# Kernel optimization log

Hardware: AMD Instinct MI355X
Metric: run time of the kernel (lower is better)

## Reference

```python
import jax, jax.numpy as jnp
import numpy as np

N, E, H = 25000, 100000, 32          # nodes, edges, node/clique hidden dim
NC, A, EC = 8000, 50000, 24000       # cliques, node2clique assignments, clique edges
EEMB, CEE, L = 8, 8, 2               # edge emb dims, n layers


def segment_mean(vals, ids, num):
    s = jax.ops.segment_sum(vals, ids, num_segments=num)
    cnt = jax.ops.segment_sum(jnp.ones(ids.shape[0], vals.dtype), ids, num_segments=num)
    return s / jnp.maximum(cnt, 1.0)[:, None]


def setup_inputs() -> dict:
    key = jax.random.key(0)
    ks = jax.random.split(key, 24)
    s = 0.1  # param scale
    inp = {
        "node_features": jax.random.normal(ks[0], (N, H), jnp.float32),
        "edge_index": jax.random.randint(ks[1], (2, E), 0, N),
        "edge_features": jax.random.normal(ks[2], (E, EEMB), jnp.float32),
        "clique_features": jax.random.normal(ks[3], (NC, H), jnp.float32),
        "node2clique_index": jnp.stack([
            jax.random.randint(ks[4], (A,), 0, N),
            jax.random.randint(ks[5], (A,), 0, NC)]),
        "clique_edge_index": jax.random.randint(ks[6], (2, EC), 0, NC),
        "clique_edge_features": jax.random.normal(ks[7], (EC, CEE), jnp.float32),
        # node NNConv params (stacked over L layers)
        "nn1_w": jax.random.normal(ks[8], (L, EEMB, H)) * s,
        "nn1_b": jnp.zeros((L, H)),
        "nn2_w": jax.random.normal(ks[9], (L, H, H * H)) * s,
        "nn2_b": jnp.zeros((L, H * H)),
        "root_w": jax.random.normal(ks[10], (L, H, H)) * s,
        "root_b": jnp.zeros((L, H)),
        # Node2Clique linear
        "n2c_w": jax.random.normal(ks[11], (L, H, H)) * s,
        "n2c_b": jnp.zeros((L, H)),
        # clique NNConv params
        "cnn1_w": jax.random.normal(ks[12], (L, CEE, H)) * s,
        "cnn1_b": jnp.zeros((L, H)),
        "cnn2_w": jax.random.normal(ks[13], (L, H, H * H)) * s,
        "cnn2_b": jnp.zeros((L, H * H)),
        "croot_w": jax.random.normal(ks[14], (L, H, H)) * s,
        "croot_b": jnp.zeros((L, H)),
        # Clique2Node linear
        "c2n_w": jax.random.normal(ks[15], (L, H, H)) * s,
        "c2n_b": jnp.zeros((L, H)),
    }
    return inp


def nnconv(x, src, dst, edge_attr, w1, b1, w2, b2, rw, rb, n_out_nodes):
    # per-edge weight matrices from the edge MLP: [E, in, out]
    h = jax.nn.relu(edge_attr @ w1 + b1)
    We = (h @ w2 + b2).reshape(edge_attr.shape[0], x.shape[1], -1)
    msg = jnp.einsum('ei,eio->eo', x[src], We)           # message from source
    agg = segment_mean(msg, dst, n_out_nodes)            # mean aggregation at target
    return agg + x @ rw + rb                             # root weight + bias


def reference(node_features, edge_index, edge_features, clique_features,
              node2clique_index, clique_edge_index, clique_edge_features,
              nn1_w, nn1_b, nn2_w, nn2_b, root_w, root_b, n2c_w, n2c_b,
              cnn1_w, cnn1_b, cnn2_w, cnn2_b, croot_w, croot_b, c2n_w, c2n_b):
    x, c = node_features, clique_features
    src, dst = edge_index[0], edge_index[1]
    nid, cid = node2clique_index[0], node2clique_index[1]
    csrc, cdst = clique_edge_index[0], clique_edge_index[1]
    for l in range(L):
        # node-level edge-conditioned conv
        x = jax.nn.relu(nnconv(x, src, dst, edge_features,
                               nn1_w[l], nn1_b[l], nn2_w[l], nn2_b[l],
                               root_w[l], root_b[l], N))
        # Node2Clique: project node feats, scatter-mean into cliques
        m = x @ n2c_w[l] + n2c_b[l]
        c = c + segment_mean(m[nid], cid, NC)
        # clique-level edge-conditioned conv
        c = jax.nn.relu(nnconv(c, csrc, cdst, clique_edge_features,
                               cnn1_w[l], cnn1_b[l], cnn2_w[l], cnn2_b[l],
                               croot_w[l], croot_b[l], NC))
        # Clique2Node: project clique feats, scatter-mean back onto nodes
        m = c @ c2n_w[l] + c2n_b[l]
        x = x + segment_mean(m[cid], nid, N)
    return (x, c)
```

## Files before the change

kernel.cpp:

```cpp
#include <hip/hip_runtime.h>
#include <hip/hip_bf16.h>

typedef unsigned int u32;
typedef unsigned short u16;

#define DEVINL __device__ __forceinline__

constexpr int Nn  = 25000;
constexpr int Ee  = 100000;
constexpr int NCc = 8000;
constexpr int Aa  = 50000;
constexpr int ECc = 24000;
constexpr int TCOLS = 1088;
constexpr int WPSZ  = TCOLS*32;
constexpr int TSP   = 1064;
constexpr int NB_N = (Nn + 255)/256;
constexpr int NB_C = (NCc + 255)/256;

typedef float f32x4 __attribute__((ext_vector_type(4)));
typedef short s16x8 __attribute__((ext_vector_type(8)));

DEVINL float b2f(u16 u){ union{u32 i;float f;}v; v.i = ((u32)u)<<16; return v.f; }
DEVINL float bfl(u32 u){ union{u32 i;float f;}v; v.i = u<<16; return v.f; }
DEVINL float bfh(u32 u){ union{u32 i;float f;}v; v.i = u & 0xffff0000u; return v.f; }
DEVINL u16 f2b(float f){ union{float f;u32 i;}v; v.f=f; u32 i=v.i;
  return (u16)((i + 0x7fffu + ((i>>16)&1u)) >> 16); }
DEVINL float ldw(const void* p, long i, int f){
  return f ? ((const float*)p)[i] : b2f(((const u16*)p)[i]);
}

__global__ __launch_bounds__(256) void k_detect(const u16* __restrict__ p, int n,
                        u32* __restrict__ maxbits, int* __restrict__ zcnt,
                        int* __restrict__ done, int* __restrict__ flag){
  int i0 = blockIdx.x*256 + threadIdx.x;
  float lm = 0.f; int lz = 0;
  for (int i = i0; i < n; i += gridDim.x*256){
    u16 v = p[i];
    if (v == 0) lz++;
    lm = fmaxf(lm, fabsf(b2f(v)));
  }
  #pragma unroll
  for (int off = 32; off; off >>= 1){
    lm = fmaxf(lm, __shfl_down(lm, off));
    lz += __shfl_down(lz, off);
  }
  if ((threadIdx.x & 63) == 0){
    atomicMax(maxbits, __float_as_uint(lm));
    atomicAdd(zcnt, lz);
  }
  __syncthreads();
  if (threadIdx.x == 0){
    __threadfence();
    if (atomicAdd(done, 1) == gridDim.x - 1){
      float m = __uint_as_float(*maxbits);
      *flag = (m > 1e6f || *zcnt > n/4) ? 1 : 0;
    }
  }
}

__global__ __launch_bounds__(256) void k_conv_all(const void* __restrict__ xin, const void* __restrict__ cin,
                         float* __restrict__ xA, float* __restrict__ cA, const int* __restrict__ flag){
  int i = blockIdx.x*256 + threadIdx.x;
  int f = *flag;
  if (i < Nn*32) xA[i] = ldw(xin, i, f);
  else { i -= Nn*32; if (i < NCc*32) cA[i] = ldw(cin, i, f); }
}

__global__ __launch_bounds__(256) void k_count_all(const int* __restrict__ ei, const int* __restrict__ cei,
                          const int* __restrict__ n2c,
                          int* __restrict__ deg_nd, int* __restrict__ deg_ce,
                          int* __restrict__ deg_n2c, int* __restrict__ deg_c2n,
                          int* __restrict__ cnt_sn, int* __restrict__ cnt_sc){
  int i = blockIdx.x*256 + threadIdx.x;
  if (i < Ee)                             atomicAdd(&deg_nd[ei[Ee + i]], 1);
  else if ((i -= Ee) < ECc)               atomicAdd(&deg_ce[cei[ECc + i]], 1);
  else if ((i -= ECc) < Aa)               atomicAdd(&deg_n2c[n2c[Aa + i]], 1);
  else if ((i -= Aa) < Aa)                atomicAdd(&deg_c2n[n2c[i]], 1);
  else if ((i -= Aa) < Ee)                atomicAdd(&cnt_sn[ei[i]], 1);
  else if ((i -= Ee) < ECc)               atomicAdd(&cnt_sc[cei[i]], 1);
}

__global__ __launch_bounds__(256) void k_scan_block(const int* __restrict__ cnt_n, const int* __restrict__ cnt_c,
                           int* __restrict__ offs_n, int* __restrict__ offs_c,
                           int* __restrict__ bsum_n, int* __restrict__ bsum_c){
  __shared__ int s[256];
  bool isC = blockIdx.x >= NB_N;
  int bid = isC ? blockIdx.x - NB_N : blockIdx.x;
  const int* cnt = isC ? cnt_c : cnt_n;
  int M = isC ? NCc : Nn;
  int tid = threadIdx.x;
  int i = bid*256 + tid;
  int v = (i < M) ? cnt[i] : 0;
  s[tid] = v; __syncthreads();
  for (int d = 1; d < 256; d <<= 1){
    int t = (tid >= d) ? s[tid-d] : 0;
    __syncthreads();
    s[tid] += t;
    __syncthreads();
  }
  if (i < M) (isC ? offs_c : offs_n)[i] = s[tid] - v;
  if (tid == 255) (isC ? bsum_c : bsum_n)[bid] = s[255];
}

__global__ __launch_bounds__(256) void k_spine(int* __restrict__ bn, int* __restrict__ bc){
  __shared__ int s[256];
  int tid = threadIdx.x;
  int v;
  if (tid < 128) v = (tid < NB_N) ? bn[tid] : 0;
  else           v = (tid-128 < NB_C) ? bc[tid-128] : 0;
  s[tid] = v; __syncthreads();
  for (int d = 1; d < 128; d <<= 1){
    int lane = tid & 127;
    int t = (lane >= d) ? s[tid-d] : 0;
    __syncthreads();
    s[tid] += t;
    __syncthreads();
  }
  if (tid < NB_N) bn[tid] = s[tid] - v;
  else if (tid >= 128 && tid-128 < NB_C) bc[tid-128] = s[tid] - v;
}

__global__ __launch_bounds__(256) void k_scan_fix(int* __restrict__ offs_n, int* __restrict__ offs_c,
                         const int* __restrict__ bn, const int* __restrict__ bc){
  int i = blockIdx.x*256 + threadIdx.x;
  if (i < Nn) offs_n[i] += bn[i >> 8];
  else if ((i -= Nn) < NCc) offs_c[i] += bc[i >> 8];
}

__global__ __launch_bounds__(256) void k_place(const int* __restrict__ ei, const int* __restrict__ cei,
                      const int* __restrict__ offs_n, const int* __restrict__ offs_c,
                      int* __restrict__ cur_n, int* __restrict__ cur_c,
                      int* __restrict__ perm_n, int* __restrict__ perm_c){
  int i = blockIdx.x*256 + threadIdx.x;
  if (i < Ee){
    int s = ei[i];
    perm_n[offs_n[s] + atomicAdd(&cur_n[s], 1)] = i;
  } else if ((i -= Ee) < ECc){
    int s = cei[i];
    perm_c[offs_c[s] + atomicAdd(&cur_c[s], 1)] = i;
  }
}

__global__ __launch_bounds__(256) void k_gather(const int* __restrict__ ei, const int* __restrict__ cei,
                       const int* __restrict__ perm_n, const int* __restrict__ perm_c,
                       const void* __restrict__ ef, const void* __restrict__ cef,
                       const int* __restrict__ flag,
                       int2* __restrict__ sdp_n, float* __restrict__ efp_n,
                       int2* __restrict__ sdp_c, float* __restrict__ efp_c){
  int i = blockIdx.x*256 + threadIdx.x;
  int f = *flag;
  if (i < Ee*8){
    int p = i >> 3, j = i & 7;
    int e = perm_n[p];
    efp_n[i] = ldw(ef, (long)e*8 + j, f);
    if (j == 0) sdp_n[p] = make_int2(ei[e], ei[Ee + e]);
  } else if ((i -= Ee*8) < ECc*8){
    int p = i >> 3, j = i & 7;
    int e = perm_c[p];
    efp_c[i] = ldw(cef, (long)e*8 + j, f);
    if (j == 0) sdp_c[p] = make_int2(cei[e], cei[ECc + e]);
  }
}

__global__ __launch_bounds__(256) void k_wpack_all(const void* __restrict__ nn2w, const void* __restrict__ nn2b,
                          const void* __restrict__ rootw,
                          const void* __restrict__ cnn2w, const void* __restrict__ cnn2b,
                          const void* __restrict__ crootw,
                          const int* __restrict__ flag, u16* __restrict__ Wp4){
  int i = blockIdx.x*256 + threadIdx.x;
  if (i >= 4*WPSZ) return;
  int set = i / WPSZ, j = i - set*WPSZ;
  int l = set >> 1, isC = set & 1;
  const void* W2 = isC ? cnn2w : nn2w;
  const void* B2 = isC ? cnn2b : nn2b;
  const void* RW = isC ? crootw : rootw;
  int f = *flag;
  int col = j >> 5, ii = j & 31;
  float v;
  if (col < 1024)      v = ldw(W2, (long)l*32768 + ((col>>5)<<10) + (ii<<5) + (col&31), f);
  else if (col < 1056) v = ldw(B2, (long)l*1024 + (ii<<5) + (col-1024), f);
  else                 v = ldw(RW, (long)l*1024 + (ii<<5) + (col-1056), f);
  Wp4[i] = f2b(v);
}

__global__ __launch_bounds__(512) void k_conv_fused(const float* __restrict__ base,
                           const float* __restrict__ addagg, const int* __restrict__ adddeg, int M,
                           const int2* __restrict__ sdp, const float* __restrict__ efp,
                           const int* __restrict__ offs, int E_,
                           const void* __restrict__ w1, long w1off,
                           const void* __restrict__ b1, long b1off,
                           const u16* __restrict__ Wp,
                           const void* __restrict__ rb, long rboff,
                           const int* __restrict__ flag,
                           float* __restrict__ feat_root, float* __restrict__ agg){
  __shared__ __align__(16) u16 Ts[16*TSP];
  __shared__ float w1s[256], b1s[32];
  __shared__ u32 hws[8][4][16];
  int tid = threadIdx.x;
  int w = tid >> 6, lane = tid & 63;
  int quad = lane >> 4, lm = lane & 15;
  int n0 = blockIdx.x * 16;
  int f = *flag;
  if (tid < 256) w1s[tid] = ldw(w1, w1off + tid, f);
  else if (tid < 288) b1s[tid-256] = ldw(b1, b1off + (tid-256), f);
  int n = n0 + lm;
  int nc = n < M ? n : M-1;
  const float* bp = base + (size_t)nc*32 + quad*8;
  s16x8 bfrag;
  if (addagg){
    int dg = adddeg[nc];
    float d = (float)(dg > 1 ? dg : 1);
    const float* ap = addagg + (size_t)nc*32 + quad*8;
    #pragma unroll
    for (int j = 0; j < 8; j++) bfrag[j] = (short)f2b(bp[j] + ap[j]/d);
  } else {
    #pragma unroll
    for (int j = 0; j < 8; j++) bfrag[j] = (short)f2b(bp[j]);
  }
  #pragma unroll 1
  for (int ti = 0; ti < 9; ti++){
    int ct = w*9 + ti;
    if (ct >= 68) break;
    int colbase = ct*16;
    s16x8 afrag = *(const s16x8*)(Wp + (size_t)(colbase + lm)*32 + quad*8);
    f32x4 acc = {0.f, 0.f, 0.f, 0.f};
    acc = __builtin_amdgcn_mfma_f32_16x16x32_bf16(afrag, bfrag, acc, 0, 0, 0);
    int cb = colbase + quad*4;
    if (ct < 66){
      u32 lo = (u32)f2b(acc[0]) | ((u32)f2b(acc[1]) << 16);
      u32 hi = (u32)f2b(acc[2]) | ((u32)f2b(acc[3]) << 16);
      *(uint2*)&Ts[lm*TSP + cb] = make_uint2(lo, hi);
    } else if (n < M){
      int o = cb - 1056;
      float4 v = make_float4(acc[0] + ldw(rb, rboff+o,   f),
                             acc[1] + ldw(rb, rboff+o+1, f),
                             acc[2] + ldw(rb, rboff+o+2, f),
                             acc[3] + ldw(rb, rboff+o+3, f));
      *(float4*)&feat_root[(size_t)n*32 + o] = v;
    }
  }
  __syncthreads();
  int lo = offs[n0];
  int n1 = n0 + 16;
  int hi = (n1 < M) ? offs[n1] : E_;
  int eg = quad, kk = lm;
  int pos = lo + w*4;
  float efv = 0.f; int sdv = 0;
  if (lane < 32){ int idx = pos*8 + lane; if (idx < hi*8) efv = efp[idx]; }
  else if (lane < 40){ int idx = pos*2 + (lane-32); if (idx < hi*2) sdv = ((const int*)sdp)[idx]; }
  for (; pos < hi; pos += 32){
    int np = pos + 32;
    float efv_n = 0.f; int sdv_n = 0;
    if (lane < 32){ int idx = np*8 + lane; if (idx < hi*8) efv_n = efp[idx]; }
    else if (lane < 40){ int idx = np*2 + (lane-32); if (idx < hi*2) sdv_n = ((const int*)sdp)[idx]; }
    int sn = __shfl(sdv, 32 + 2*eg);
    int dn = __shfl(sdv, 33 + 2*eg);
    bool valid = (pos + eg < hi);
    int sr = sn - n0; sr = sr < 0 ? 0 : (sr > 15 ? 15 : sr);
    float a0 = b1s[2*kk], a1 = b1s[2*kk+1];
    #pragma unroll
    for (int j = 0; j < 8; j++){
      float ev = __shfl(efv, eg*8 + j);
      a0 += ev * w1s[j*32 + 2*kk];
      a1 += ev * w1s[j*32 + 2*kk+1];
    }
    hws[w][eg][kk] = (u32)f2b(fmaxf(a0, 0.f)) | ((u32)f2b(fmaxf(a1, 0.f)) << 16);
    if (valid){
      const u16* Tr = &Ts[sr*TSP];
      u32 vb = *(const u32*)&Tr[1024 + 2*kk];
      float m0 = bfl(vb), m1 = bfh(vb);
      #pragma unroll
      for (int kq = 0; kq < 16; kq++){
        u32 hp = hws[w][eg][kq];
        float h0 = bfl(hp), h1 = bfh(hp);
        u32 v0 = *(const u32*)&Tr[(2*kq)*32 + 2*kk];
        u32 v1 = *(const u32*)&Tr[(2*kq+1)*32 + 2*kk];
        m0 += h0*bfl(v0) + h1*bfl(v1);
        m1 += h0*bfh(v0) + h1*bfh(v1);
      }
      float* ap = agg + (size_t)dn*32 + 2*kk;
      atomicAdd(ap,   m0);
      atomicAdd(ap+1, m1);
    }
    efv = efv_n; sdv = sdv_n;
  }
}

__global__ __launch_bounds__(256) void k_update_lin(const float* __restrict__ agg, const int* __restrict__ deg,
                           const float* __restrict__ feat_root, int M,
                           const void* __restrict__ w, long woff,
                           const void* __restrict__ b, long boff,
                           const int* __restrict__ flag,
                           float* __restrict__ feat, float* __restrict__ m_out){
  __shared__ float wsm[1024], bs[32], rows[8][33];
  int tid = threadIdx.x;
  int f = *flag;
  for (int idx = tid; idx < 1024; idx += 256) wsm[idx] = ldw(w, woff + idx, f);
  if (tid < 32) bs[tid] = ldw(b, boff + tid, f);
  int nl = tid >> 5, o = tid & 31;
  int n = blockIdx.x*8 + nl;
  if (n < M){
    int dg = deg[n];
    float d = (float)(dg > 1 ? dg : 1);
    float v = fmaxf(agg[(size_t)n*32 + o]/d + feat_root[(size_t)n*32 + o], 0.f);
    rows[nl][o] = v;
    feat[(size_t)n*32 + o] = v;
  }
  __syncthreads();
  if (n >= M) return;
  float acc = bs[o];
  #pragma unroll
  for (int j = 0; j < 32; j++) acc += rows[nl][j]*wsm[j*32+o];
  m_out[(size_t)n*32 + o] = acc;
}

__global__ __launch_bounds__(256) void k_scatter(const int* __restrict__ gidx, const int* __restrict__ sidx, int A_,
                          const float* __restrict__ m, float* __restrict__ agg){
  int i = blockIdx.x*256 + threadIdx.x;
  if (i >= A_*32) return;
  int a = i >> 5, o = i & 31;
  atomicAdd(&agg[(size_t)sidx[a]*32 + o], m[(size_t)gidx[a]*32 + o]);
}

__global__ __launch_bounds__(256) void k_store(const float* __restrict__ x, const float* __restrict__ xagg,
                      const int* __restrict__ xdeg, const float* __restrict__ c,
                      void* __restrict__ out, const int* __restrict__ flag){
  int i = blockIdx.x*256 + threadIdx.x;
  int tot = Nn*32 + NCc*32;
  if (i >= tot) return;
  float v;
  if (i < Nn*32){
    int n = i >> 5;
    int dg = xdeg[n];
    float d = (float)(dg > 1 ? dg : 1);
    v = x[i] + xagg[i]/d;
  } else v = c[i - Nn*32];
  if (*flag) ((float*)out)[i] = v;
  else       ((u16*)out)[i]   = f2b(v);
}

extern "C" void kernel_launch(void* const* d_in, const int* in_sizes, int n_in,
                              void* d_out, int out_size, void* d_ws, size_t ws_size,
                              hipStream_t stream){
  const int* ei  = (const int*)d_in[1];
  const int* n2c = (const int*)d_in[4];
  const int* cei = (const int*)d_in[5];
  const void *efr = d_in[2], *cefr = d_in[6];
  const void *nn1w = d_in[7], *nn1b = d_in[8], *nn2w = d_in[9], *nn2b = d_in[10],
             *rootw = d_in[11], *rootb = d_in[12], *n2cw = d_in[13], *n2cb = d_in[14],
             *cnn1w = d_in[15], *cnn1b = d_in[16], *cnn2w = d_in[17], *cnn2b = d_in[18],
             *crootw = d_in[19], *crootb = d_in[20], *c2nw = d_in[21], *c2nb = d_in[22];

  char* ws = (char*)d_ws;
  size_t off = 0;
  auto alloc = [&](size_t bytes){ void* p = ws + off; off += (bytes + 255) & ~(size_t)255; return p; };

  size_t zstart = off;
  float *aggE[2], *caggS[2], *caggE[2], *aggS[2];
  for (int l = 0; l < 2; l++){
    aggE[l]  = (float*)alloc((size_t)Nn*32*4);
    caggS[l] = (float*)alloc((size_t)NCc*32*4);
    caggE[l] = (float*)alloc((size_t)NCc*32*4);
    aggS[l]  = (float*)alloc((size_t)Nn*32*4);
  }
  int* deg_nd  = (int*)alloc((size_t)Nn*4);
  int* deg_ce  = (int*)alloc((size_t)NCc*4);
  int* deg_n2c = (int*)alloc((size_t)NCc*4);
  int* deg_c2n = (int*)alloc((size_t)Nn*4);
  int* cnt_sn  = (int*)alloc((size_t)Nn*4);
  int* cnt_sc  = (int*)alloc((size_t)NCc*4);
  int* cur_n   = (int*)alloc((size_t)Nn*4);
  int* cur_c   = (int*)alloc((size_t)NCc*4);
  u32* maxbits = (u32*)alloc(256);
  int* zcnt = (int*)((char*)maxbits + 4);
  int* flag = (int*)((char*)maxbits + 8);
  int* done = (int*)((char*)maxbits + 12);
  size_t zbytes = off - zstart;

  float* xA  = (float*)alloc((size_t)Nn*32*4);
  float* xB  = (float*)alloc((size_t)Nn*32*4);
  float* xC  = (float*)alloc((size_t)Nn*32*4);
  float* cA  = (float*)alloc((size_t)NCc*32*4);
  float* cC0 = (float*)alloc((size_t)NCc*32*4);
  float* cC1 = (float*)alloc((size_t)NCc*32*4);
  float* m   = (float*)alloc((size_t)Nn*32*4);
  float* frn = (float*)alloc((size_t)Nn*32*4);
  float* frc = (float*)alloc((size_t)NCc*32*4);
  int* offs_n = (int*)alloc((size_t)Nn*4);
  int* offs_c = (int*)alloc((size_t)NCc*4);
  int* bsum_n = (int*)alloc(512);
  int* bsum_c = (int*)alloc(512);
  int* perm_n = (int*)alloc((size_t)Ee*4);
  int* perm_c = (int*)alloc((size_t)ECc*4);
  int2* sdp_n = (int2*)alloc((size_t)Ee*8);
  int2* sdp_c = (int2*)alloc((size_t)ECc*8);
  float* efp_n = (float*)alloc((size_t)Ee*8*4);
  float* efp_c = (float*)alloc((size_t)ECc*8*4);
  u16* Wp4 = (u16*)alloc((size_t)4*WPSZ*2);

  auto nb = [](int n){ return (n + 255)/256; };

  hipMemsetAsync(ws + zstart, 0, zbytes, stream);
  k_detect<<<256,256,0,stream>>>((const u16*)d_in[0], Nn*32, maxbits, zcnt, done, flag);
  k_conv_all<<<nb(Nn*32 + NCc*32),256,0,stream>>>(d_in[0], d_in[3], xA, cA, flag);
  k_count_all<<<nb(2*Ee + 2*ECc + 2*Aa),256,0,stream>>>(ei, cei, n2c,
      deg_nd, deg_ce, deg_n2c, deg_c2n, cnt_sn, cnt_sc);
  k_scan_block<<<NB_N+NB_C,256,0,stream>>>(cnt_sn, cnt_sc, offs_n, offs_c, bsum_n, bsum_c);
  k_spine<<<1,256,0,stream>>>(bsum_n, bsum_c);
  k_scan_fix<<<nb(Nn+NCc),256,0,stream>>>(offs_n, offs_c, bsum_n, bsum_c);
  k_place<<<nb(Ee+ECc),256,0,stream>>>(ei, cei, offs_n, offs_c, cur_n, cur_c, perm_n, perm_c);
  k_gather<<<nb(8*(Ee+ECc)),256,0,stream>>>(ei, cei, perm_n, perm_c, efr, cefr, flag,
      sdp_n, efp_n, sdp_c, efp_c);
  k_wpack_all<<<nb(4*WPSZ),256,0,stream>>>(nn2w, nn2b, rootw, cnn2w, cnn2b, crootw, flag, Wp4);

  int Gn = (Nn + 15)/16, Gc = (NCc + 15)/16;

  k_conv_fused<<<Gn,512,0,stream>>>(xA, nullptr, nullptr, Nn, sdp_n, efp_n, offs_n, Ee,
      nn1w, 0, nn1b, 0, Wp4 + 0*WPSZ, rootb, 0, flag, frn, aggE[0]);
  k_update_lin<<<(Nn+7)/8,256,0,stream>>>(aggE[0], deg_nd, frn, Nn, n2cw, 0, n2cb, 0, flag, xB, m);
  k_scatter<<<nb(Aa*32),256,0,stream>>>(n2c, n2c+Aa, Aa, m, caggS[0]);
  k_conv_fused<<<Gc,512,0,stream>>>(cA, caggS[0], deg_n2c, NCc, sdp_c, efp_c, offs_c, ECc,
      cnn1w, 0, cnn1b, 0, Wp4 + 1*WPSZ, crootb, 0, flag, frc, caggE[0]);
  k_update_lin<<<(NCc+7)/8,256,0,stream>>>(caggE[0], deg_ce, frc, NCc, c2nw, 0, c2nb, 0, flag, cC0, m);
  k_scatter<<<nb(Aa*32),256,0,stream>>>(n2c+Aa, n2c, Aa, m, aggS[0]);
  k_conv_fused<<<Gn,512,0,stream>>>(xB, aggS[0], deg_c2n, Nn, sdp_n, efp_n, offs_n, Ee,
      nn1w, 256, nn1b, 32, Wp4 + 2*WPSZ, rootb, 32, flag, frn, aggE[1]);
  k_update_lin<<<(Nn+7)/8,256,0,stream>>>(aggE[1], deg_nd, frn, Nn, n2cw, 1024, n2cb, 32, flag, xC, m);
  k_scatter<<<nb(Aa*32),256,0,stream>>>(n2c, n2c+Aa, Aa, m, caggS[1]);
  k_conv_fused<<<Gc,512,0,stream>>>(cC0, caggS[1], deg_n2c, NCc, sdp_c, efp_c, offs_c, ECc,
      cnn1w, 256, cnn1b, 32, Wp4 + 3*WPSZ, crootb, 32, flag, frc, caggE[1]);
  k_update_lin<<<(NCc+7)/8,256,0,stream>>>(caggE[1], deg_ce, frc, NCc, c2nw, 1024, c2nb, 32, flag, cC1, m);
  k_scatter<<<nb(Aa*32),256,0,stream>>>(n2c+Aa, n2c, Aa, m, aggS[1]);
  k_store<<<nb(Nn*32 + NCc*32),256,0,stream>>>(xC, aggS[1], deg_c2n, cC1, d_out, flag);
}
```

Before: 347.3 us.

## Replace atomic scatter-mean with CSR segment-mean and restructure conv smem layout

Builds CSR indices for node-to-clique and clique-to-node assignments (extra scan segments and placement) so the scatter-mean steps become deterministic gather-based segment means with no atomics. Those kernels also apply the residual add, which removes the add-aggregate path from the conv kernel. The conv kernel's shared-memory tile is re-laid out as packed u32 with a new stride, allowing 128-bit vector reads in the message loop. Edge-feature prefetch is deepened to two iterations ahead. In exchange there is more preprocessing work, and the per-thread serial loops in the segment-mean kernels may suffer from load imbalance.

```diff
diff --git a/kernel.cpp b/kernel.cpp
--- a/kernel.cpp
+++ b/kernel.cpp
@@ -13,7 +13,7 @@
 constexpr int ECc = 24000;
 constexpr int TCOLS = 1088;
 constexpr int WPSZ  = TCOLS*32;
-constexpr int TSP   = 1064;
+constexpr int NSTR  = 580;
 constexpr int NB_N = (Nn + 255)/256;
 constexpr int NB_C = (NCc + 255)/256;
 
@@ -25,6 +25,7 @@
 DEVINL float bfh(u32 u){ union{u32 i;float f;}v; v.i = u & 0xffff0000u; return v.f; }
 DEVINL u16 f2b(float f){ union{float f;u32 i;}v; v.f=f; u32 i=v.i;
   return (u16)((i + 0x7fffu + ((i>>16)&1u)) >> 16); }
+DEVINL u32 pk2(float a, float b){ return (u32)f2b(a) | ((u32)f2b(b) << 16); }
 DEVINL float ldw(const void* p, long i, int f){
   return f ? ((const float*)p)[i] : b2f(((const u16*)p)[i]);
 }
@@ -80,16 +81,23 @@
   else if ((i -= Ee) < ECc)               atomicAdd(&cnt_sc[cei[i]], 1);
 }
 
-__global__ __launch_bounds__(256) void k_scan_block(const int* __restrict__ cnt_n, const int* __restrict__ cnt_c,
-                           int* __restrict__ offs_n, int* __restrict__ offs_c,
-                           int* __restrict__ bsum_n, int* __restrict__ bsum_c){
+__global__ __launch_bounds__(256) void k_scan_block(
+    const int* __restrict__ c0, const int* __restrict__ c1,
+    const int* __restrict__ c2, const int* __restrict__ c3,
+    int* __restrict__ o0, int* __restrict__ o1, int* __restrict__ o2, int* __restrict__ o3,
+    int* __restrict__ b0, int* __restrict__ b1, int* __restrict__ b2, int* __restrict__ b3){
   __shared__ int s[256];
-  bool isC = blockIdx.x >= NB_N;
-  int bid = isC ? blockIdx.x - NB_N : blockIdx.x;
-  const int* cnt = isC ? cnt_c : cnt_n;
-  int M = isC ? NCc : Nn;
+  int bid = blockIdx.x, seg, rb;
+  if (bid < NB_N){ seg=0; rb=bid; }
+  else if (bid < NB_N+NB_C){ seg=1; rb=bid-NB_N; }
+  else if (bid < 2*NB_N+NB_C){ seg=2; rb=bid-NB_N-NB_C; }
+  else { seg=3; rb=bid-2*NB_N-NB_C; }
+  const int* cnt = seg==0?c0 : seg==1?c1 : seg==2?c2 : c3;
+  int* offs = seg==0?o0 : seg==1?o1 : seg==2?o2 : o3;
+  int* bs   = seg==0?b0 : seg==1?b1 : seg==2?b2 : b3;
+  int M = (seg & 1) ? NCc : Nn;
   int tid = threadIdx.x;
-  int i = bid*256 + tid;
+  int i = rb*256 + tid;
   int v = (i < M) ? cnt[i] : 0;
   s[tid] = v; __syncthreads();
   for (int d = 1; d < 256; d <<= 1){
@@ -98,39 +106,46 @@
     s[tid] += t;
     __syncthreads();
   }
-  if (i < M) (isC ? offs_c : offs_n)[i] = s[tid] - v;
-  if (tid == 255) (isC ? bsum_c : bsum_n)[bid] = s[255];
-}
-
-__global__ __launch_bounds__(256) void k_spine(int* __restrict__ bn, int* __restrict__ bc){
-  __shared__ int s[256];
-  int tid = threadIdx.x;
-  int v;
-  if (tid < 128) v = (tid < NB_N) ? bn[tid] : 0;
-  else           v = (tid-128 < NB_C) ? bc[tid-128] : 0;
+  if (i < M) offs[i] = s[tid] - v;
+  if (tid == 255) bs[rb] = s[255];
+}
+
+__global__ __launch_bounds__(512) void k_spine(int* __restrict__ b0, int* __restrict__ b1,
+                      int* __restrict__ b2, int* __restrict__ b3){
+  __shared__ int s[512];
+  int tid = threadIdx.x, seg = tid >> 7, lane = tid & 127;
+  int NB = (seg & 1) ? NB_C : NB_N;
+  int* bp = seg==0?b0 : seg==1?b1 : seg==2?b2 : b3;
+  int v = (lane < NB) ? bp[lane] : 0;
   s[tid] = v; __syncthreads();
   for (int d = 1; d < 128; d <<= 1){
-    int lane = tid & 127;
     int t = (lane >= d) ? s[tid-d] : 0;
     __syncthreads();
     s[tid] += t;
     __syncthreads();
   }
-  if (tid < NB_N) bn[tid] = s[tid] - v;
-  else if (tid >= 128 && tid-128 < NB_C) bc[tid-128] = s[tid] - v;
-}
-
-__global__ __launch_bounds__(256) void k_scan_fix(int* __restrict__ offs_n, int* __restrict__ offs_c,
-                         const int* __restrict__ bn, const int* __restrict__ bc){
-  int i = blockIdx.x*256 + threadIdx.x;
-  if (i < Nn) offs_n[i] += bn[i >> 8];
-  else if ((i -= Nn) < NCc) offs_c[i] += bc[i >> 8];
+  if (lane < NB) bp[lane] = s[tid] - v;
+}
+
+__global__ __launch_bounds__(256) void k_scan_fix(
+    int* __restrict__ o0, int* __restrict__ o1, int* __restrict__ o2, int* __restrict__ o3,
+    const int* __restrict__ b0, const int* __restrict__ b1,
+    const int* __restrict__ b2, const int* __restrict__ b3){
+  int i = blockIdx.x*256 + threadIdx.x;
+  if (i < Nn) o0[i] += b0[i >> 8];
+  else if ((i -= Nn) < NCc) o1[i] += b1[i >> 8];
+  else if ((i -= NCc) < Nn) o2[i] += b2[i >> 8];
+  else if ((i -= Nn) < NCc) o3[i] += b3[i >> 8];
 }
 
 __global__ __launch_bounds__(256) void k_place(const int* __restrict__ ei, const int* __restrict__ cei,
+                      const int* __restrict__ n2c,
                       const int* __restrict__ offs_n, const int* __restrict__ offs_c,
+                      const int* __restrict__ offs_an, const int* __restrict__ offs_ac,
                       int* __restrict__ cur_n, int* __restrict__ cur_c,
-                      int* __restrict__ perm_n, int* __restrict__ perm_c){
+                      int* __restrict__ cur_an, int* __restrict__ cur_ac,
+                      int* __restrict__ perm_n, int* __restrict__ perm_c,
+                      int* __restrict__ an2c, int* __restrict__ ac2n){
   int i = blockIdx.x*256 + threadIdx.x;
   if (i < Ee){
     int s = ei[i];
@@ -138,6 +153,12 @@
   } else if ((i -= Ee) < ECc){
     int s = cei[i];
     perm_c[offs_c[s] + atomicAdd(&cur_c[s], 1)] = i;
+  } else if ((i -= ECc) < Aa){
+    int c = n2c[Aa + i];
+    an2c[offs_ac[c] + atomicAdd(&cur_ac[c], 1)] = n2c[i];
+  } else if ((i -= Aa) < Aa){
+    int nd = n2c[i];
+    ac2n[offs_an[nd] + atomicAdd(&cur_an[nd], 1)] = n2c[Aa + i];
   }
 }
 
@@ -183,8 +204,7 @@
   Wp4[i] = f2b(v);
 }
 
-__global__ __launch_bounds__(512) void k_conv_fused(const float* __restrict__ base,
-                           const float* __restrict__ addagg, const int* __restrict__ adddeg, int M,
+__global__ __launch_bounds__(512) void k_conv_fused(const float* __restrict__ base, int M,
                            const int2* __restrict__ sdp, const float* __restrict__ efp,
                            const int* __restrict__ offs, int E_,
                            const void* __restrict__ w1, long w1off,
@@ -193,30 +213,23 @@
                            const void* __restrict__ rb, long rboff,
                            const int* __restrict__ flag,
                            float* __restrict__ feat_root, float* __restrict__ agg){
-  __shared__ __align__(16) u16 Ts[16*TSP];
-  __shared__ float w1s[256], b1s[32];
-  __shared__ u32 hws[8][4][16];
+  __shared__ __align__(16) u32 Ts[16*NSTR];
+  __shared__ float w1s[256];
+  __shared__ __align__(8) u32 hws[8][4][16];
   int tid = threadIdx.x;
   int w = tid >> 6, lane = tid & 63;
   int quad = lane >> 4, lm = lane & 15;
   int n0 = blockIdx.x * 16;
   int f = *flag;
   if (tid < 256) w1s[tid] = ldw(w1, w1off + tid, f);
-  else if (tid < 288) b1s[tid-256] = ldw(b1, b1off + (tid-256), f);
+  float bb0 = ldw(b1, b1off + 2*lm, f);
+  float bb1 = ldw(b1, b1off + 2*lm + 1, f);
   int n = n0 + lm;
   int nc = n < M ? n : M-1;
   const float* bp = base + (size_t)nc*32 + quad*8;
   s16x8 bfrag;
-  if (addagg){
-    int dg = adddeg[nc];
-    float d = (float)(dg > 1 ? dg : 1);
-    const float* ap = addagg + (size_t)nc*32 + quad*8;
-    #pragma unroll
-    for (int j = 0; j < 8; j++) bfrag[j] = (short)f2b(bp[j] + ap[j]/d);
-  } else {
-    #pragma unroll
-    for (int j = 0; j < 8; j++) bfrag[j] = (short)f2b(bp[j]);
-  }
+  #pragma unroll
+  for (int j = 0; j < 8; j++) bfrag[j] = (short)f2b(bp[j]);
   #pragma unroll 1
   for (int ti = 0; ti < 9; ti++){
     int ct = w*9 + ti;
@@ -225,13 +238,15 @@
     s16x8 afrag = *(const s16x8*)(Wp + (size_t)(colbase + lm)*32 + quad*8);
     f32x4 acc = {0.f, 0.f, 0.f, 0.f};
     acc = __builtin_amdgcn_mfma_f32_16x16x32_bf16(afrag, bfrag, acc, 0, 0, 0);
-    int cb = colbase + quad*4;
     if (ct < 66){
-      u32 lo = (u32)f2b(acc[0]) | ((u32)f2b(acc[1]) << 16);
-      u32 hi = (u32)f2b(acc[2]) | ((u32)f2b(acc[3]) << 16);
-      *(uint2*)&Ts[lm*TSP + cb] = make_uint2(lo, hi);
+      int k = ct >> 1;
+      int p0 = (ct & 1)*8 + quad*2;
+      int idx = lm*NSTR + p0*36 + k;
+      Ts[idx]      = pk2(acc[0], acc[1]);
+      Ts[idx + 36] = pk2(acc[2], acc[3]);
     } else if (n < M){
-      int o = cb - 1056;
+      int o = (ct - 66)*16 + quad*4 - 0;
+      o = (colbase + quad*4) - 1056;
       float4 v = make_float4(acc[0] + ldw(rb, rboff+o,   f),
                              acc[1] + ldw(rb, rboff+o+1, f),
                              acc[2] + ldw(rb, rboff+o+2, f),
@@ -241,48 +256,51 @@
   }
   __syncthreads();
   int lo = offs[n0];
-  int n1 = n0 + 16;
-  int hi = (n1 < M) ? offs[n1] : E_;
+  int hi = (n0 + 16 < M) ? offs[n0 + 16] : E_;
   int eg = quad, kk = lm;
   int pos = lo + w*4;
-  float efv = 0.f; int sdv = 0;
-  if (lane < 32){ int idx = pos*8 + lane; if (idx < hi*8) efv = efp[idx]; }
-  else if (lane < 40){ int idx = pos*2 + (lane-32); if (idx < hi*2) sdv = ((const int*)sdp)[idx]; }
+  float ef0 = 0.f, ef1 = 0.f; int sd0 = 0, sd1 = 0;
+  if (lane < 32){
+    int idx = pos*8 + lane;        if (idx < hi*8) ef0 = efp[idx];
+    idx = (pos+32)*8 + lane;       if (idx < hi*8) ef1 = efp[idx];
+  } else if (lane < 40){
+    int idx = pos*2 + (lane-32);   if (idx < hi*2) sd0 = ((const int*)sdp)[idx];
+    idx = (pos+32)*2 + (lane-32);  if (idx < hi*2) sd1 = ((const int*)sdp)[idx];
+  }
   for (; pos < hi; pos += 32){
-    int np = pos + 32;
-    float efv_n = 0.f; int sdv_n = 0;
-    if (lane < 32){ int idx = np*8 + lane; if (idx < hi*8) efv_n = efp[idx]; }
-    else if (lane < 40){ int idx = np*2 + (lane-32); if (idx < hi*2) sdv_n = ((const int*)sdp)[idx]; }
-    int sn = __shfl(sdv, 32 + 2*eg);
-    int dn = __shfl(sdv, 33 + 2*eg);
+    int np = pos + 64;
+    float ef2 = 0.f; int sd2 = 0;
+    if (lane < 32){ int idx = np*8 + lane; if (idx < hi*8) ef2 = efp[idx]; }
+    else if (lane < 40){ int idx = np*2 + (lane-32); if (idx < hi*2) sd2 = ((const int*)sdp)[idx]; }
+    int sn = __shfl(sd0, 32 + 2*eg);
+    int dn = __shfl(sd0, 33 + 2*eg);
     bool valid = (pos + eg < hi);
     int sr = sn - n0; sr = sr < 0 ? 0 : (sr > 15 ? 15 : sr);
-    float a0 = b1s[2*kk], a1 = b1s[2*kk+1];
+    float a0 = bb0, a1 = bb1;
     #pragma unroll
     for (int j = 0; j < 8; j++){
-      float ev = __shfl(efv, eg*8 + j);
+      float ev = __shfl(ef0, eg*8 + j);
       a0 += ev * w1s[j*32 + 2*kk];
       a1 += ev * w1s[j*32 + 2*kk+1];
     }
-    hws[w][eg][kk] = (u32)f2b(fmaxf(a0, 0.f)) | ((u32)f2b(fmaxf(a1, 0.f)) << 16);
+    hws[w][eg][kk] = pk2(fmaxf(a0, 0.f), fmaxf(a1, 0.f));
     if (valid){
-      const u16* Tr = &Ts[sr*TSP];
-      u32 vb = *(const u32*)&Tr[1024 + 2*kk];
+      const u32* Tr = &Ts[sr*NSTR + kk*36];
+      u32 vb = Tr[32];
       float m0 = bfl(vb), m1 = bfh(vb);
       #pragma unroll
-      for (int kq = 0; kq < 16; kq++){
-        u32 hp = hws[w][eg][kq];
-        float h0 = bfl(hp), h1 = bfh(hp);
-        u32 v0 = *(const u32*)&Tr[(2*kq)*32 + 2*kk];
-        u32 v1 = *(const u32*)&Tr[(2*kq+1)*32 + 2*kk];
-        m0 += h0*bfl(v0) + h1*bfl(v1);
-        m1 += h0*bfh(v0) + h1*bfh(v1);
+      for (int g = 0; g < 8; g++){
+        uint4 tv = *(const uint4*)&Tr[g*4];
+        uint2 hp = *(const uint2*)&hws[w][eg][g*2];
+        float h0 = bfl(hp.x), h1 = bfh(hp.x), h2 = bfl(hp.y), h3 = bfh(hp.y);
+        m0 += h0*bfl(tv.x) + h1*bfl(tv.y) + h2*bfl(tv.z) + h3*bfl(tv.w);
+        m1 += h0*bfh(tv.x) + h1*bfh(tv.y) + h2*bfh(tv.z) + h3*bfh(tv.w);
       }
       float* ap = agg + (size_t)dn*32 + 2*kk;
       atomicAdd(ap,   m0);
       atomicAdd(ap+1, m1);
     }
-    efv = efv_n; sdv = sdv_n;
+    ef0 = ef1; sd0 = sd1; ef1 = ef2; sd1 = sd2;
   }
 }
 
@@ -291,7 +309,8 @@
                            const void* __restrict__ w, long woff,
                            const void* __restrict__ b, long boff,
                            const int* __restrict__ flag,
-                           float* __restrict__ feat, float* __restrict__ m_out){
+                           float* __restrict__ feat, void* __restrict__ dt_out, long dt_off,
+                           float* __restrict__ m_out){
   __shared__ float wsm[1024], bs[32], rows[8][33];
   int tid = threadIdx.x;
   int f = *flag;
@@ -299,42 +318,49 @@
   if (tid < 32) bs[tid] = ldw(b, boff + tid, f);
   int nl = tid >> 5, o = tid & 31;
   int n = blockIdx.x*8 + nl;
+  long i = (long)n*32 + o;
   if (n < M){
     int dg = deg[n];
     float d = (float)(dg > 1 ? dg : 1);
-    float v = fmaxf(agg[(size_t)n*32 + o]/d + feat_root[(size_t)n*32 + o], 0.f);
+    float v = fmaxf(agg[i]/d + feat_root[i], 0.f);
     rows[nl][o] = v;
-    feat[(size_t)n*32 + o] = v;
+    if (feat) feat[i] = v;
+    if (dt_out){
+      if (f) ((float*)dt_out)[dt_off + i] = v;
+      else   ((u16*)dt_out)[dt_off + i]   = f2b(v);
+    }
   }
   __syncthreads();
   if (n >= M) return;
   float acc = bs[o];
   #pragma unroll
   for (int j = 0; j < 32; j++) acc += rows[nl][j]*wsm[j*32+o];
-  m_out[(size_t)n*32 + o] = acc;
-}
-
-__global__ __launch_bounds__(256) void k_scatter(const int* __restrict__ gidx, const int* __restrict__ sidx, int A_,
-                          const float* __restrict__ m, float* __restrict__ agg){
-  int i = blockIdx.x*256 + threadIdx.x;
-  if (i >= A_*32) return;
-  int a = i >> 5, o = i & 31;
-  atomicAdd(&agg[(size_t)sidx[a]*32 + o], m[(size_t)gidx[a]*32 + o]);
-}
-
-__global__ __launch_bounds__(256) void k_store(const float* __restrict__ x, const float* __restrict__ xagg,
-                      const int* __restrict__ xdeg, const float* __restrict__ c,
-                      void* __restrict__ out, const int* __restrict__ flag){
-  int i = blockIdx.x*256 + threadIdx.x;
-  int tot = Nn*32 + NCc*32;
-  if (i >= tot) return;
-  float v;
-  if (i < Nn*32){
-    int n = i >> 5;
-    int dg = xdeg[n];
-    float d = (float)(dg > 1 ? dg : 1);
-    v = x[i] + xagg[i]/d;
-  } else v = c[i - Nn*32];
+  m_out[i] = acc;
+}
+
+__global__ __launch_bounds__(256) void k_segmean(const float* __restrict__ base, const float* __restrict__ m,
+                        const int* __restrict__ idxarr, const int* __restrict__ offs,
+                        const int* __restrict__ deg, int M, float* __restrict__ out){
+  int i = blockIdx.x*256 + threadIdx.x;
+  if (i >= M*32) return;
+  int c = i >> 5, o = i & 31;
+  int lo = offs[c], cnt = deg[c];
+  float s = 0.f;
+  for (int a = lo; a < lo + cnt; a++) s += m[(size_t)idxarr[a]*32 + o];
+  out[i] = base[i] + s/(float)(cnt > 1 ? cnt : 1);
+}
+
+__global__ __launch_bounds__(256) void k_segmean_out(const float* __restrict__ base, const float* __restrict__ m,
+                        const int* __restrict__ idxarr, const int* __restrict__ offs,
+                        const int* __restrict__ deg, int M,
+                        void* __restrict__ out, const int* __restrict__ flag){
+  int i = blockIdx.x*256 + threadIdx.x;
+  if (i >= M*32) return;
+  int c = i >> 5, o = i & 31;
+  int lo = offs[c], cnt = deg[c];
+  float s = 0.f;
+  for (int a = lo; a < lo + cnt; a++) s += m[(size_t)idxarr[a]*32 + o];
+  float v = base[i] + s/(float)(cnt > 1 ? cnt : 1);
   if (*flag) ((float*)out)[i] = v;
   else       ((u16*)out)[i]   = f2b(v);
 }
@@ -356,13 +382,10 @@
   auto alloc = [&](size_t bytes){ void* p = ws + off; off += (bytes + 255) & ~(size_t)255; return p; };
 
   size_t zstart = off;
-  float *aggE[2], *caggS[2], *caggE[2], *aggS[2];
-  for (int l = 0; l < 2; l++){
-    aggE[l]  = (float*)alloc((size_t)Nn*32*4);
-    caggS[l] = (float*)alloc((size_t)NCc*32*4);
-    caggE[l] = (float*)alloc((size_t)NCc*32*4);
-    aggS[l]  = (float*)alloc((size_t)Nn*32*4);
-  }
+  float* aggE0  = (float*)alloc((size_t)Nn*32*4);
+  float* aggE1  = (float*)alloc((size_t)Nn*32*4);
+  float* caggE0 = (float*)alloc((size_t)NCc*32*4);
+  float* caggE1 = (float*)alloc((size_t)NCc*32*4);
   int* deg_nd  = (int*)alloc((size_t)Nn*4);
   int* deg_ce  = (int*)alloc((size_t)NCc*4);
   int* deg_n2c = (int*)alloc((size_t)NCc*4);
@@ -371,6 +394,8 @@
   int* cnt_sc  = (int*)alloc((size_t)NCc*4);
   int* cur_n   = (int*)alloc((size_t)Nn*4);
   int* cur_c   = (int*)alloc((size_t)NCc*4);
+  int* cur_an  = (int*)alloc((size_t)Nn*4);
+  int* cur_ac  = (int*)alloc((size_t)NCc*4);
   u32* maxbits = (u32*)alloc(256);
   int* zcnt = (int*)((char*)maxbits + 4);
   int* flag = (int*)((char*)maxbits + 8);
@@ -379,19 +404,28 @@
 
   float* xA  = (float*)alloc((size_t)Nn*32*4);
   float* xB  = (float*)alloc((size_t)Nn*32*4);
+  float* xA1 = (float*)alloc((size_t)Nn*32*4);
   float* xC  = (float*)alloc((size_t)Nn*32*4);
   float* cA  = (float*)alloc((size_t)NCc*32*4);
+  float* cB  = (float*)alloc((size_t)NCc*32*4);
   float* cC0 = (float*)alloc((size_t)NCc*32*4);
-  float* cC1 = (float*)alloc((size_t)NCc*32*4);
-  float* m   = (float*)alloc((size_t)Nn*32*4);
+  float* cB1 = (float*)alloc((size_t)NCc*32*4);
+  float* m_n = (float*)alloc((size_t)Nn*32*4);
+  float* m_c = (float*)alloc((size_t)NCc*32*4);
   float* frn = (float*)alloc((size_t)Nn*32*4);
   float* frc = (float*)alloc((size_t)NCc*32*4);
-  int* offs_n = (int*)alloc((size_t)Nn*4);
-  int* offs_c = (int*)alloc((size_t)NCc*4);
-  int* bsum_n = (int*)alloc(512);
-  int* bsum_c = (int*)alloc(512);
+  int* offs_n  = (int*)alloc((size_t)Nn*4);
+  int* offs_c  = (int*)alloc((size_t)NCc*4);
+  int* offs_an = (int*)alloc((size_t)Nn*4);
+  int* offs_ac = (int*)alloc((size_t)NCc*4);
+  int* bsum0 = (int*)alloc(512);
+  int* bsum1 = (int*)alloc(512);
+  int* bsum2 = (int*)alloc(512);
+  int* bsum3 = (int*)alloc(512);
   int* perm_n = (int*)alloc((size_t)Ee*4);
   int* perm_c = (int*)alloc((size_t)ECc*4);
+  int* an2c = (int*)alloc((size_t)Aa*4);
+  int* ac2n = (int*)alloc((size_t)Aa*4);
   int2* sdp_n = (int2*)alloc((size_t)Ee*8);
   int2* sdp_c = (int2*)alloc((size_t)ECc*8);
   float* efp_n = (float*)alloc((size_t)Ee*8*4);
@@ -405,31 +439,37 @@
   k_conv_all<<<nb(Nn*32 + NCc*32),256,0,stream>>>(d_in[0], d_in[3], xA, cA, flag);
   k_count_all<<<nb(2*Ee + 2*ECc + 2*Aa),256,0,stream>>>(ei, cei, n2c,
       deg_nd, deg_ce, deg_n2c, deg_c2n, cnt_sn, cnt_sc);
-  k_scan_block<<<NB_N+NB_C,256,0,stream>>>(cnt_sn, cnt_sc, offs_n, offs_c, bsum_n, bsum_c);
-  k_spine<<<1,256,0,stream>>>(bsum_n, bsum_c);
-  k_scan_fix<<<nb(Nn+NCc),256,0,stream>>>(offs_n, offs_c, bsum_n, bsum_c);
-  k_place<<<nb(Ee+ECc),256,0,stream>>>(ei, cei, offs_n, offs_c, cur_n, cur_c, perm_n, perm_c);
+  k_scan_block<<<2*(NB_N+NB_C),256,0,stream>>>(cnt_sn, cnt_sc, deg_c2n, deg_n2c,
+      offs_n, offs_c, offs_an, offs_ac, bsum0, bsum1, bsum2, bsum3);
+  k_spine<<<1,512,0,stream>>>(bsum0, bsum1, bsum2, bsum3);
+  k_scan_fix<<<nb(2*(Nn+NCc)),256,0,stream>>>(offs_n, offs_c, offs_an, offs_ac,
+      bsum0, bsum1, bsum2, bsum3);
+  k_place<<<nb(Ee+ECc+2*Aa),256,0,stream>>>(ei, cei, n2c, offs_n, offs_c, offs_an, offs_ac,
+      cur_n, cur_c, cur_an, cur_ac, perm_n, perm_c, an2c, ac2n);
   k_gather<<<nb(8*(Ee+ECc)),256,0,stream>>>(ei, cei, perm_n, perm_c, efr, cefr, flag,
       sdp_n, efp_n, sdp_c, efp_c);
   k_wpack_all<<<nb(4*WPSZ),256,0,stream>>>(nn2w, nn2b, rootw, cnn2w, cnn2b, crootw, flag, Wp4);
 
   int Gn = (Nn + 15)/16, Gc = (NCc + 15)/16;
 
-  k_conv_fused<<<Gn,512,0,stream>>>(xA, nullptr, nullptr, Nn, sdp_n, efp_n, offs_n, Ee,
-      nn1w, 0, nn1b, 0, Wp4 + 0*WPSZ, rootb, 0, flag, frn, aggE[0]);
-  k_update_lin<<<(Nn+7)/8,256,0,stream>>>(aggE[0], deg_nd, frn, Nn, n2cw, 0, n2cb, 0, flag, xB, m);
-  k_scatter<<<nb(Aa*32),256,0,stream>>>(n2c, n2c+Aa, Aa, m, caggS[0]);
-  k_conv_fused<<<Gc,512,0,stream>>>(cA, caggS[0], deg_n2c, NCc, sdp_c, efp_c, offs_c, ECc,
-      cnn1w, 0, cnn1b, 0, Wp4 + 1*WPSZ, crootb, 0, flag, frc, caggE[0]);
-  k_update_lin<<<(NCc+7)/8,256,0,stream>>>(caggE[0], deg_ce, frc, NCc, c2nw, 0, c2nb, 0, flag, cC0, m);
-  k_scatter<<<nb(Aa*32),256,0,stream>>>(n2c+Aa, n2c, Aa, m, aggS[0]);
-  k_conv_fused<<<Gn,512,0,stream>>>(xB, aggS[0], deg_c2n, Nn, sdp_n, efp_n, offs_n, Ee,
-      nn1w, 256, nn1b, 32, Wp4 + 2*WPSZ, rootb, 32, flag, frn, aggE[1]);
-  k_update_lin<<<(Nn+7)/8,256,0,stream>>>(aggE[1], deg_nd, frn, Nn, n2cw, 1024, n2cb, 32, flag, xC, m);
-  k_scatter<<<nb(Aa*32),256,0,stream>>>(n2c, n2c+Aa, Aa, m, caggS[1]);
-  k_conv_fused<<<Gc,512,0,stream>>>(cC0, caggS[1], deg_n2c, NCc, sdp_c, efp_c, offs_c, ECc,
-      cnn1w, 256, cnn1b, 32, Wp4 + 3*WPSZ, crootb, 32, flag, frc, caggE[1]);
-  k_update_lin<<<(NCc+7)/8,256,0,stream>>>(caggE[1], deg_ce, frc, NCc, c2nw, 1024, c2nb, 32, flag, cC1, m);
-  k_scatter<<<nb(Aa*32),256,0,stream>>>(n2c+Aa, n2c, Aa, m, aggS[1]);
-  k_store<<<nb(Nn*32 + NCc*32),256,0,stream>>>(xC, aggS[1], deg_c2n, cC1, d_out, flag);
-}
+  k_conv_fused<<<Gn,512,0,stream>>>(xA, Nn, sdp_n, efp_n, offs_n, Ee,
+      nn1w, 0, nn1b, 0, Wp4 + 0*WPSZ, rootb, 0, flag, frn, aggE0);
+  k_update_lin<<<(Nn+7)/8,256,0,stream>>>(aggE0, deg_nd, frn, Nn, n2cw, 0, n2cb, 0, flag,
+      xB, nullptr, 0, m_n);
+  k_segmean<<<nb(NCc*32),256,0,stream>>>(cA, m_n, an2c, offs_ac, deg_n2c, NCc, cB);
+  k_conv_fused<<<Gc,512,0,stream>>>(cB, NCc, sdp_c, efp_c, offs_c, ECc,
+      cnn1w, 0, cnn1b, 0, Wp4 + 1*WPSZ, crootb, 0, flag, frc, caggE0);
+  k_update_lin<<<(NCc+7)/8,256,0,stream>>>(caggE0, deg_ce, frc, NCc, c2nw, 0, c2nb, 0, flag,
+      cC0, nullptr, 0, m_c);
+  k_segmean<<<nb(Nn*32),256,0,stream>>>(xB, m_c, ac2n, offs_an, deg_c2n, Nn, xA1);
+  k_conv_fused<<<Gn,512,0,stream>>>(xA1, Nn, sdp_n, efp_n, offs_n, Ee,
+      nn1w, 256, nn1b, 32, Wp4 + 2*WPSZ, rootb, 32, flag, frn, aggE1);
+  k_update_lin<<<(Nn+7)/8,256,0,stream>>>(aggE1, deg_nd, frn, Nn, n2cw, 1024, n2cb, 32, flag,
+      xC, nullptr, 0, m_n);
+  k_segmean<<<nb(NCc*32),256,0,stream>>>(cC0, m_n, an2c, offs_ac, deg_n2c, NCc, cB1);
+  k_conv_fused<<<Gc,512,0,stream>>>(cB1, NCc, sdp_c, efp_c, offs_c, ECc,
+      cnn1w, 256, cnn1b, 32, Wp4 + 3*WPSZ, crootb, 32, flag, frc, caggE1);
+  k_update_lin<<<(NCc+7)/8,256,0,stream>>>(caggE1, deg_ce, frc, NCc, c2nw, 1024, c2nb, 32, flag,
+      nullptr, d_out, (long)Nn*32, m_c);
+  k_segmean_out<<<nb(Nn*32),256,0,stream>>>(xC, m_c, ac2n, offs_an, deg_c2n, Nn, d_out, flag);
+}
```

Measured after the change: 351.1 us. About the same (+1.1%).
